# Kernel tuning notes

Hardware: AMD Instinct MI355X
Metric: run time of the kernel (lower is better)

The kernel has to match this reference:

```python
import jax, jax.numpy as jnp
import numpy as np

N_HEADS = 16
EMB_DIM = 1024
HEAD_DIM = EMB_DIM // N_HEADS


def setup_inputs() -> dict:
    key = jax.random.key(0)
    k1, k2, k3, k4, k5 = jax.random.split(key, 5)
    s = 1.0 / np.sqrt(EMB_DIM)
    return {
        "attn_in": jax.random.normal(k1, (4, 2048, EMB_DIM), dtype=jnp.float32),
        "W_qkv": jax.random.uniform(k2, (EMB_DIM, 3 * EMB_DIM), jnp.float32, -s, s),
        "b_qkv": jax.random.uniform(k3, (3 * EMB_DIM,), jnp.float32, -s, s),
        "W_out": jax.random.uniform(k4, (EMB_DIM, EMB_DIM), jnp.float32, -s, s),
        "b_out": jax.random.uniform(k5, (EMB_DIM,), jnp.float32, -s, s),
    }


def reference(attn_in, W_qkv, b_qkv, W_out, b_out):
    N, L, E = attn_in.shape
    qkv = attn_in @ W_qkv + b_qkv                      # [N, L, 3E]
    q, k, v = jnp.split(qkv, 3, axis=-1)
    # [N, L, E] -> [N, H, L, D]
    def heads(x):
        return x.reshape(N, L, N_HEADS, HEAD_DIM).transpose(0, 2, 1, 3)
    q, k, v = heads(q), heads(k), heads(v)
    scale = 1.0 / np.sqrt(HEAD_DIM)
    scores = jnp.einsum('nhqd,nhkd->nhqk', q, k) * scale   # [N, H, L, L]
    attn = jax.nn.softmax(scores, axis=-1)
    o = jnp.einsum('nhqk,nhkd->nhqd', attn, v)             # [N, H, L, D]
    o = o.transpose(0, 2, 1, 3).reshape(N, L, E)
    return o @ W_out + b_out
```

## Files before the change

kernel.cpp:

```cpp
#include <hip/hip_runtime.h>

typedef __attribute__((ext_vector_type(8))) short short8;
typedef __attribute__((ext_vector_type(4))) float f32x4;

#define MFMA16(A,B,C) __builtin_amdgcn_mfma_f32_16x16x32_bf16(A,B,C,0,0,0)

__device__ __forceinline__ short f2bf(float f){
  union { float f; unsigned int u; } v; v.f = f;
  unsigned int u = v.u;
  unsigned int r = (u + 0x7fffu + ((u >> 16) & 1u)) >> 16;
  return (short)r;
}

typedef const __attribute__((address_space(1))) void* gptr_t;
typedef __attribute__((address_space(3))) void* lptr_t;

__device__ __forceinline__ void gload16(const short* g, short* l){
  __builtin_amdgcn_global_load_lds((gptr_t)g, (lptr_t)l, 16, 0, 0);
}


__global__ __launch_bounds__(256) void cvt_x_kernel(const float* __restrict__ x,
                                                    short* __restrict__ xb){
  const size_t i = (size_t)blockIdx.x * 256 + threadIdx.x;
  const float4* p = (const float4*)x + i * 2;
  float4 a = p[0], b = p[1];
  short8 o;
  o[0]=f2bf(a.x); o[1]=f2bf(a.y); o[2]=f2bf(a.z); o[3]=f2bf(a.w);
  o[4]=f2bf(b.x); o[5]=f2bf(b.y); o[6]=f2bf(b.z); o[7]=f2bf(b.w);
  *(short8*)(xb + i * 8) = o;
}

__global__ __launch_bounds__(256) void cvt_t_kernel(const float* __restrict__ src,
                                                    short* __restrict__ dst,
                                                    int R, int C){
  __shared__ float tile[32][33];
  const int tx = threadIdx.x, ty = threadIdx.y;
  const int c0 = blockIdx.x * 32, r0 = blockIdx.y * 32;
  #pragma unroll
  for (int i = 0; i < 32; i += 8)
    tile[ty + i][tx] = src[(size_t)(r0 + ty + i) * C + c0 + tx];
  __syncthreads();
  #pragma unroll
  for (int i = 0; i < 32; i += 8)
    dst[(size_t)(c0 + ty + i) * R + r0 + tx] = f2bf(tile[tx][ty + i]);
}


template<int EPI>
__global__ __launch_bounds__(256) void gemm_bt(
    const short* __restrict__ A, const short* __restrict__ BT,
    const float* __restrict__ bias,
    float* __restrict__ Cf,
    short* __restrict__ q_ws, short* __restrict__ k_ws, short* __restrict__ vt_ws)
{
  __shared__ __align__(16) short As[4096];
  __shared__ __align__(16) short Bs[4096];
  const int tid = threadIdx.x;
  const int bm = blockIdx.x, bn = blockIdx.y;
  const int lane = tid & 63, wid = tid >> 6;
  const int wr = wid >> 1, wc = wid & 1;
  const int r = lane & 15, g = lane >> 4;

  f32x4 acc[4][4] = {};

  const short* ag = A  + (size_t)(bm * 128 + (tid >> 2)) * 1024 + (tid & 3) * 8;
  const short* bg = BT + (size_t)(bn * 128 + (tid >> 2)) * 1024 + (tid & 3) * 8;
  short* asd = &As[tid * 8];
  short* bsd = &Bs[tid * 8];

  for (int kk = 0; kk < 32; ++kk){
    gload16(ag + kk * 32,             asd);
    gload16(ag + kk * 32 + 64 * 1024, asd + 2048);
    gload16(bg + kk * 32,             bsd);
    gload16(bg + kk * 32 + 64 * 1024, bsd + 2048);
    asm volatile("s_waitcnt vmcnt(0)" ::: "memory");
    __syncthreads();
    short8 a[4], b[4];
    #pragma unroll
    for (int mf = 0; mf < 4; ++mf)
      a[mf] = *(const short8*)&As[(wr * 64 + mf * 16 + r) * 32 + g * 8];
    #pragma unroll
    for (int nf = 0; nf < 4; ++nf)
      b[nf] = *(const short8*)&Bs[(wc * 64 + nf * 16 + r) * 32 + g * 8];
    #pragma unroll
    for (int mf = 0; mf < 4; ++mf)
      #pragma unroll
      for (int nf = 0; nf < 4; ++nf)
        acc[mf][nf] = MFMA16(a[mf], b[nf], acc[mf][nf]);
    __syncthreads();
  }

  if (EPI == 0){
    #pragma unroll
    for (int nf = 0; nf < 4; ++nf){
      const int c = bn * 128 + wc * 64 + nf * 16 + r;
      const float bv = bias[c];
      const int type = c >> 10;
      const int h = (c & 1023) >> 6, d = c & 63;
      const float mul = (type == 0) ? 0.18033688011112042f : 1.0f;
      #pragma unroll
      for (int mf = 0; mf < 4; ++mf){
        const int row0 = bm * 128 + wr * 64 + mf * 16 + g * 4;
        const int nb = row0 >> 11, l0 = row0 & 2047;
        f32x4 v = acc[mf][nf];
        if (type == 2){
          short4 pk;
          pk.x = f2bf(v[0] + bv); pk.y = f2bf(v[1] + bv);
          pk.z = f2bf(v[2] + bv); pk.w = f2bf(v[3] + bv);
          *(short4*)&vt_ws[((size_t)(nb * 16 + h) * 64 + d) * 2048 + l0] = pk;
        } else {
          short* dst = (type == 0) ? q_ws : k_ws;
          const size_t base = ((size_t)(nb * 16 + h) * 2048 + l0) * 64 + d;
          #pragma unroll
          for (int j = 0; j < 4; ++j)
            dst[base + (size_t)j * 64] = f2bf((v[j] + bv) * mul);
        }
      }
    }
  } else {
    #pragma unroll
    for (int nf = 0; nf < 4; ++nf){
      const int c = bn * 128 + wc * 64 + nf * 16 + r;
      const float bv = bias[c];
      #pragma unroll
      for (int mf = 0; mf < 4; ++mf){
        const int row0 = bm * 128 + wr * 64 + mf * 16 + g * 4;
        f32x4 v = acc[mf][nf];
        #pragma unroll
        for (int j = 0; j < 4; ++j)
          Cf[(size_t)(row0 + j) * 1024 + c] = v[j] + bv;
      }
    }
  }
}


__global__ __launch_bounds__(512, 4) void attn_kernel(
    const short* __restrict__ qw, const short* __restrict__ kw,
    const short* __restrict__ vtw, short* __restrict__ ow)
{
  __shared__ __align__(16) short Ks[3][4096];
  __shared__ __align__(16) short Vs[3][4096];
  __shared__ __align__(16) short Pb[8][2][1024];

  const int id = blockIdx.x;
  const int xcd = id & 7, j2 = id >> 3;
  const int nh = xcd * 8 + (j2 & 7);
  const int qt = j2 >> 3;
  const int tid = threadIdx.x;
  const int lane = tid & 63, w = tid >> 6;
  const int r = lane & 15, g = lane >> 4;
  const int rx = (r & 7) << 3;

  const size_t hoff = (size_t)nh * 2048 * 64;
  const short* kh = kw + hoff;
  const short* vh = vtw + hoff;

  const int srow = tid >> 3, sc = tid & 7;
  const int sswz = (sc * 8) ^ ((srow & 7) << 3);
  const short* ksrc = kh + srow * 64 + sswz;
  const short* vsrc = vh + (size_t)srow * 2048 + sswz;

  short* pK0 = &Ks[0][0]; short* pK1 = &Ks[1][0]; short* pK2 = &Ks[2][0];
  short* pV0 = &Vs[0][0]; short* pV1 = &Vs[1][0]; short* pV2 = &Vs[2][0];

  const int qrow0 = qt * 256 + w * 32;
  short8 qfr[2][2];
  #pragma unroll
  for (int qf = 0; qf < 2; ++qf)
    #pragma unroll
    for (int hh = 0; hh < 2; ++hh)
      qfr[qf][hh] = *(const short8*)(qw + hoff +
          (size_t)(qrow0 + qf * 16 + r) * 64 + hh * 32 + g * 8);

  f32x4 oa[2][4] = {};
  f32x4 lacc[2] = {};
  short8 ones;
  #pragma unroll
  for (int i = 0; i < 8; ++i) ones[i] = (short)0x3F80;

  short* Pq[2] = { &Pb[w][0][0], &Pb[w][1][0] };

  gload16(ksrc,        pK0 + tid * 8);
  gload16(vsrc,        pV0 + tid * 8);
  gload16(ksrc + 4096, pK1 + tid * 8);
  gload16(vsrc + 64,   pV1 + tid * 8);

  for (int kt = 0; kt < 32; ++kt){
    asm volatile("s_waitcnt vmcnt(2)" ::: "memory");
    __builtin_amdgcn_s_barrier();
    {
      const int ts = (kt + 2) & 31;
      gload16(ksrc + ts * 4096, pK2 + tid * 8);
      gload16(vsrc + ts * 64,   pV2 + tid * 8);
    }

    f32x4 ss[2][4];
    #pragma unroll
    for (int qf = 0; qf < 2; ++qf)
      #pragma unroll
      for (int cb = 0; cb < 4; ++cb)
        ss[qf][cb] = f32x4{0.f, 0.f, 0.f, 0.f};
    #pragma unroll
    for (int cb = 0; cb < 4; ++cb){
      const int rbase = (cb * 16 + r) * 64;
      short8 kf0 = *(const short8*)&pK0[rbase + ((g * 8) ^ rx)];
      short8 kf1 = *(const short8*)&pK0[rbase + ((32 + g * 8) ^ rx)];
      ss[0][cb] = MFMA16(kf0, qfr[0][0], ss[0][cb]);
      ss[0][cb] = MFMA16(kf1, qfr[0][1], ss[0][cb]);
      ss[1][cb] = MFMA16(kf0, qfr[1][0], ss[1][cb]);
      ss[1][cb] = MFMA16(kf1, qfr[1][1], ss[1][cb]);
    }

    #pragma unroll
    for (int qf = 0; qf < 2; ++qf){
      #pragma unroll
      for (int cb = 0; cb < 4; ++cb){
        float p0 = exp2f(ss[qf][cb][0]);
        float p1 = exp2f(ss[qf][cb][1]);
        float p2 = exp2f(ss[qf][cb][2]);
        float p3 = exp2f(ss[qf][cb][3]);
        unsigned int w0, w1;
        asm("v_cvt_pk_bf16_f32 %0, %1, %2" : "=v"(w0) : "v"(p0), "v"(p1));
        asm("v_cvt_pk_bf16_f32 %0, %1, %2" : "=v"(w1) : "v"(p2), "v"(p3));
        uint2 u; u.x = w0; u.y = w1;
        *(uint2*)&Pq[qf][r * 64 + ((cb * 16 + g * 4) ^ rx)] = u;
      }
    }

    __builtin_amdgcn_wave_barrier();

    #pragma unroll
    for (int ka = 0; ka < 2; ++ka){
      const int kcol = (ka * 32 + g * 8) ^ rx;
      short8 pa0 = *(const short8*)&Pq[0][r * 64 + kcol];
      short8 pa1 = *(const short8*)&Pq[1][r * 64 + kcol];
      #pragma unroll
      for (int db = 0; db < 4; ++db){
        short8 vf = *(const short8*)&pV0[(db * 16 + r) * 64 + kcol];
        oa[0][db] = MFMA16(pa0, vf, oa[0][db]);
        oa[1][db] = MFMA16(pa1, vf, oa[1][db]);
      }
      lacc[0] = MFMA16(pa0, ones, lacc[0]);
      lacc[1] = MFMA16(pa1, ones, lacc[1]);
    }
    __builtin_amdgcn_wave_barrier();

    short* tk = pK0; pK0 = pK1; pK1 = pK2; pK2 = tk;
    short* tv = pV0; pV0 = pV1; pV1 = pV2; pV2 = tv;
  }

  const int n = nh >> 4, h = nh & 15;
  #pragma unroll
  for (int qf = 0; qf < 2; ++qf){
    float invb[4];
    #pragma unroll
    for (int j = 0; j < 4; ++j) invb[j] = 1.0f / lacc[qf][j];
    #pragma unroll
    for (int db = 0; db < 4; ++db)
      #pragma unroll
      for (int j = 0; j < 4; ++j){
        const float val = oa[qf][db][j] * invb[j];
        ow[((size_t)n * 2048 + qrow0 + qf * 16 + g * 4 + j) * 1024 + h * 64 + db * 16 + r]
          = f2bf(val);
      }
  }
}


extern "C" void kernel_launch(void* const* d_in, const int* in_sizes, int n_in,
                              void* d_out, int out_size, void* d_ws, size_t ws_size,
                              hipStream_t stream){
  const float* attn_in = (const float*)d_in[0];
  const float* W_qkv   = (const float*)d_in[1];
  const float* b_qkv   = (const float*)d_in[2];
  const float* W_out   = (const float*)d_in[3];
  const float* b_out   = (const float*)d_in[4];
  float* out = (float*)d_out;

  char* ws = (char*)d_ws;
  short* xb    = (short*)(ws);
  short* wqT   = (short*)(ws + 16777216);
  short* woT   = (short*)(ws + 23068672);
  short* q_ws  = (short*)(ws + 25165824);
  short* k_ws  = (short*)(ws + 41943040);
  short* vt_ws = (short*)(ws + 58720256);
  short* o_ws  = (short*)(ws + 75497472);

  cvt_x_kernel<<<4096, 256, 0, stream>>>(attn_in, xb);
  cvt_t_kernel<<<dim3(96, 32), dim3(32, 8), 0, stream>>>(W_qkv, wqT, 1024, 3072);
  cvt_t_kernel<<<dim3(32, 32), dim3(32, 8), 0, stream>>>(W_out, woT, 1024, 1024);
  gemm_bt<0><<<dim3(64, 24), 256, 0, stream>>>(xb, wqT, b_qkv, nullptr, q_ws, k_ws, vt_ws);
  attn_kernel<<<512, 512, 0, stream>>>(q_ws, k_ws, vt_ws, o_ws);
  gemm_bt<1><<<dim3(64, 8), 256, 0, stream>>>(o_ws, woT, b_out, out, nullptr, nullptr, nullptr);
}
```

Before: 208.0 us.

## Switch attention to 32x32 MFMA with register-resident P via permlane swap

Rewrites the attention inner loop to use 32x32x16 bf16 MFMA instead of 16x16x32. The softmax probabilities are kept in registers and rearranged with v_permlane32_swap into the A-operand layout, which removes the per-wave LDS round-trip for P and its wave barriers. The K/V ring buffer grows from 3 to 4 stages with prefetch distance 3, and the loop is unrolled by 4 so buffer indices are static. This uses more LDS for K/V but none for P, and it changes accumulator register pressure and the output store pattern.

```diff
diff --git a/kernel.cpp b/kernel.cpp
--- a/kernel.cpp
+++ b/kernel.cpp
@@ -2,8 +2,10 @@
 
 typedef __attribute__((ext_vector_type(8))) short short8;
 typedef __attribute__((ext_vector_type(4))) float f32x4;
+typedef __attribute__((ext_vector_type(16))) float f32x16;
 
 #define MFMA16(A,B,C) __builtin_amdgcn_mfma_f32_16x16x32_bf16(A,B,C,0,0,0)
+#define MFMA32(A,B,C) __builtin_amdgcn_mfma_f32_32x32x16_bf16(A,B,C,0,0,0)
 
 __device__ __forceinline__ short f2bf(float f){
   union { float f; unsigned int u; } v; v.f = f;
@@ -140,9 +142,8 @@
     const short* __restrict__ qw, const short* __restrict__ kw,
     const short* __restrict__ vtw, short* __restrict__ ow)
 {
-  __shared__ __align__(16) short Ks[3][4096];
-  __shared__ __align__(16) short Vs[3][4096];
-  __shared__ __align__(16) short Pb[8][2][1024];
+  __shared__ __align__(16) short Ks[4][4096];
+  __shared__ __align__(16) short Vs[4][4096];
 
   const int id = blockIdx.x;
   const int xcd = id & 7, j2 = id >> 3;
@@ -150,121 +151,115 @@
   const int qt = j2 >> 3;
   const int tid = threadIdx.x;
   const int lane = tid & 63, w = tid >> 6;
-  const int r = lane & 15, g = lane >> 4;
-  const int rx = (r & 7) << 3;
+  const int l31 = lane & 31, hi = lane >> 5, w7 = lane & 7;
 
   const size_t hoff = (size_t)nh * 2048 * 64;
   const short* kh = kw + hoff;
   const short* vh = vtw + hoff;
 
-  const int srow = tid >> 3, sc = tid & 7;
-  const int sswz = (sc * 8) ^ ((srow & 7) << 3);
-  const short* ksrc = kh + srow * 64 + sswz;
-  const short* vsrc = vh + (size_t)srow * 2048 + sswz;
-
-  short* pK0 = &Ks[0][0]; short* pK1 = &Ks[1][0]; short* pK2 = &Ks[2][0];
-  short* pV0 = &Vs[0][0]; short* pV1 = &Vs[1][0]; short* pV2 = &Vs[2][0];
+  const int srow = tid >> 3, schunk = tid & 7;
+  const int scw = (schunk ^ (srow & 7)) * 8;
+  const short* ksrc = kh + srow * 64 + scw;
+  const short* vsrc = vh + (size_t)srow * 2048 + scw;
+
+  unsigned aoffh[2][4];
+  #pragma unroll
+  for (int T = 0; T < 2; ++T)
+    #pragma unroll
+    for (int s = 0; s < 4; ++s)
+      aoffh[T][s] = (unsigned)((l31 + 32 * T) * 64 + (((2 * s + hi) ^ w7) * 8));
 
   const int qrow0 = qt * 256 + w * 32;
-  short8 qfr[2][2];
-  #pragma unroll
-  for (int qf = 0; qf < 2; ++qf)
-    #pragma unroll
-    for (int hh = 0; hh < 2; ++hh)
-      qfr[qf][hh] = *(const short8*)(qw + hoff +
-          (size_t)(qrow0 + qf * 16 + r) * 64 + hh * 32 + g * 8);
-
-  f32x4 oa[2][4] = {};
-  f32x4 lacc[2] = {};
-  short8 ones;
-  #pragma unroll
-  for (int i = 0; i < 8; ++i) ones[i] = (short)0x3F80;
-
-  short* Pq[2] = { &Pb[w][0][0], &Pb[w][1][0] };
-
-  gload16(ksrc,        pK0 + tid * 8);
-  gload16(vsrc,        pV0 + tid * 8);
-  gload16(ksrc + 4096, pK1 + tid * 8);
-  gload16(vsrc + 64,   pV1 + tid * 8);
-
-  for (int kt = 0; kt < 32; ++kt){
-    asm volatile("s_waitcnt vmcnt(2)" ::: "memory");
-    __builtin_amdgcn_s_barrier();
-    {
-      const int ts = (kt + 2) & 31;
-      gload16(ksrc + ts * 4096, pK2 + tid * 8);
-      gload16(vsrc + ts * 64,   pV2 + tid * 8);
+  short8 qfr[4];
+  #pragma unroll
+  for (int s = 0; s < 4; ++s)
+    qfr[s] = *(const short8*)(qw + hoff + (size_t)(qrow0 + l31) * 64 + s * 16 + hi * 8);
+
+  f32x16 oa0 = {}, oa1 = {}, lacc = {};
+  short8 onesB;
+  #pragma unroll
+  for (int i = 0; i < 8; ++i) onesB[i] = (short)0x3F80;
+
+  gload16(ksrc,        &Ks[0][tid * 8]);
+  gload16(vsrc,        &Vs[0][tid * 8]);
+  gload16(ksrc + 4096, &Ks[1][tid * 8]);
+  gload16(vsrc + 64,   &Vs[1][tid * 8]);
+  gload16(ksrc + 8192, &Ks[2][tid * 8]);
+  gload16(vsrc + 128,  &Vs[2][tid * 8]);
+
+  for (int t4 = 0; t4 < 32; t4 += 4){
+    #pragma unroll
+    for (int u = 0; u < 4; ++u){
+      const int t = t4 + u;
+      asm volatile("s_waitcnt vmcnt(4)" ::: "memory");
+      __builtin_amdgcn_s_barrier();
+      {
+        const int ts = (t + 3) & 31;
+        gload16(ksrc + ts * 4096, &Ks[(u + 3) & 3][tid * 8]);
+        gload16(vsrc + ts * 64,   &Vs[(u + 3) & 3][tid * 8]);
+      }
+      const short* Kb = &Ks[u][0];
+      const short* Vb = &Vs[u][0];
+
+      f32x16 ss0, ss1;
+      {
+        short8 k0 = *(const short8*)&Kb[aoffh[0][0]];
+        short8 k1 = *(const short8*)&Kb[aoffh[1][0]];
+        const f32x16 zz = {};
+        ss0 = MFMA32(k0, qfr[0], zz);
+        ss1 = MFMA32(k1, qfr[0], zz);
+      }
+      #pragma unroll
+      for (int s = 1; s < 4; ++s){
+        short8 k0 = *(const short8*)&Kb[aoffh[0][s]];
+        short8 k1 = *(const short8*)&Kb[aoffh[1][s]];
+        ss0 = MFMA32(k0, qfr[s], ss0);
+        ss1 = MFMA32(k1, qfr[s], ss1);
+      }
+
+      unsigned u0[8], u1[8];
+      #pragma unroll
+      for (int m = 0; m < 8; ++m){
+        float a = exp2f(ss0[2 * m]), b = exp2f(ss0[2 * m + 1]);
+        asm("v_cvt_pk_bf16_f32 %0, %1, %2" : "=v"(u0[m]) : "v"(a), "v"(b));
+        float c = exp2f(ss1[2 * m]), d = exp2f(ss1[2 * m + 1]);
+        asm("v_cvt_pk_bf16_f32 %0, %1, %2" : "=v"(u1[m]) : "v"(c), "v"(d));
+      }
+
+      short8 pa[4];
+      #pragma unroll
+      for (int s = 0; s < 4; ++s){
+        const int sg = (s & 1) * 4;
+        unsigned a0 = (s < 2) ? u0[sg + 0] : u1[sg + 0];
+        unsigned a1 = (s < 2) ? u0[sg + 1] : u1[sg + 1];
+        unsigned a2 = (s < 2) ? u0[sg + 2] : u1[sg + 2];
+        unsigned a3 = (s < 2) ? u0[sg + 3] : u1[sg + 3];
+        asm("v_permlane32_swap_b32 %0, %1" : "+v"(a0), "+v"(a2));
+        asm("v_permlane32_swap_b32 %0, %1" : "+v"(a1), "+v"(a3));
+        union { unsigned q[4]; short8 s8; } cv;
+        cv.q[0] = a0; cv.q[1] = a1; cv.q[2] = a2; cv.q[3] = a3;
+        pa[s] = cv.s8;
+      }
+
+      #pragma unroll
+      for (int s = 0; s < 4; ++s){
+        short8 v0 = *(const short8*)&Vb[aoffh[0][s]];
+        short8 v1 = *(const short8*)&Vb[aoffh[1][s]];
+        oa0 = MFMA32(pa[s], v0, oa0);
+        oa1 = MFMA32(pa[s], v1, oa1);
+        lacc = MFMA32(pa[s], onesB, lacc);
+      }
     }
-
-    f32x4 ss[2][4];
-    #pragma unroll
-    for (int qf = 0; qf < 2; ++qf)
-      #pragma unroll
-      for (int cb = 0; cb < 4; ++cb)
-        ss[qf][cb] = f32x4{0.f, 0.f, 0.f, 0.f};
-    #pragma unroll
-    for (int cb = 0; cb < 4; ++cb){
-      const int rbase = (cb * 16 + r) * 64;
-      short8 kf0 = *(const short8*)&pK0[rbase + ((g * 8) ^ rx)];
-      short8 kf1 = *(const short8*)&pK0[rbase + ((32 + g * 8) ^ rx)];
-      ss[0][cb] = MFMA16(kf0, qfr[0][0], ss[0][cb]);
-      ss[0][cb] = MFMA16(kf1, qfr[0][1], ss[0][cb]);
-      ss[1][cb] = MFMA16(kf0, qfr[1][0], ss[1][cb]);
-      ss[1][cb] = MFMA16(kf1, qfr[1][1], ss[1][cb]);
-    }
-
-    #pragma unroll
-    for (int qf = 0; qf < 2; ++qf){
-      #pragma unroll
-      for (int cb = 0; cb < 4; ++cb){
-        float p0 = exp2f(ss[qf][cb][0]);
-        float p1 = exp2f(ss[qf][cb][1]);
-        float p2 = exp2f(ss[qf][cb][2]);
-        float p3 = exp2f(ss[qf][cb][3]);
-        unsigned int w0, w1;
-        asm("v_cvt_pk_bf16_f32 %0, %1, %2" : "=v"(w0) : "v"(p0), "v"(p1));
-        asm("v_cvt_pk_bf16_f32 %0, %1, %2" : "=v"(w1) : "v"(p2), "v"(p3));
-        uint2 u; u.x = w0; u.y = w1;
-        *(uint2*)&Pq[qf][r * 64 + ((cb * 16 + g * 4) ^ rx)] = u;
-      }
-    }
-
-    __builtin_amdgcn_wave_barrier();
-
-    #pragma unroll
-    for (int ka = 0; ka < 2; ++ka){
-      const int kcol = (ka * 32 + g * 8) ^ rx;
-      short8 pa0 = *(const short8*)&Pq[0][r * 64 + kcol];
-      short8 pa1 = *(const short8*)&Pq[1][r * 64 + kcol];
-      #pragma unroll
-      for (int db = 0; db < 4; ++db){
-        short8 vf = *(const short8*)&pV0[(db * 16 + r) * 64 + kcol];
-        oa[0][db] = MFMA16(pa0, vf, oa[0][db]);
-        oa[1][db] = MFMA16(pa1, vf, oa[1][db]);
-      }
-      lacc[0] = MFMA16(pa0, ones, lacc[0]);
-      lacc[1] = MFMA16(pa1, ones, lacc[1]);
-    }
-    __builtin_amdgcn_wave_barrier();
-
-    short* tk = pK0; pK0 = pK1; pK1 = pK2; pK2 = tk;
-    short* tv = pV0; pV0 = pV1; pV1 = pV2; pV2 = tv;
   }
 
   const int n = nh >> 4, h = nh & 15;
   #pragma unroll
-  for (int qf = 0; qf < 2; ++qf){
-    float invb[4];
-    #pragma unroll
-    for (int j = 0; j < 4; ++j) invb[j] = 1.0f / lacc[qf][j];
-    #pragma unroll
-    for (int db = 0; db < 4; ++db)
-      #pragma unroll
-      for (int j = 0; j < 4; ++j){
-        const float val = oa[qf][db][j] * invb[j];
-        ow[((size_t)n * 2048 + qrow0 + qf * 16 + g * 4 + j) * 1024 + h * 64 + db * 16 + r]
-          = f2bf(val);
-      }
+  for (int j = 0; j < 16; ++j){
+    const float inv = 1.0f / lacc[j];
+    const int qr = (j & 3) + 8 * (j >> 2) + 4 * hi;
+    const size_t base = ((size_t)n * 2048 + qrow0 + qr) * 1024 + h * 64 + l31;
+    ow[base]      = f2bf(oa0[j] * inv);
+    ow[base + 32] = f2bf(oa1[j] * inv);
   }
 }
 
```

Result: no change. 208.3 us (+0.1%).
